# Kernel tuning notes

Hardware: AMD Instinct MI355X
Metric: run time of the kernel (lower is better)

The kernel has to match this reference:

```python
import jax, jax.numpy as jnp
import numpy as np

EMB, QK, V, H = 1024, 64, 64, 16
B, S = 4, 2048


def setup_inputs() -> dict:
    key = jax.random.key(0)
    ks = jax.random.split(key, 8)
    sc = 0.02
    x_q = jax.random.normal(ks[0], (B, S, EMB), jnp.float32)
    x_k_v = jax.random.normal(ks[1], (B, S, EMB), jnp.float32)
    # causal mask: True means masked (matches torch masked_fill)
    causal = ~jnp.tril(jnp.ones((S, S), dtype=bool))
    attn_mask = jnp.broadcast_to(causal, (B, S, S))
    w_q = jax.random.normal(ks[2], (H * QK, EMB), jnp.float32) * sc
    b_q = jnp.zeros((H * QK,), jnp.float32)
    w_k = jax.random.normal(ks[3], (H * QK, EMB), jnp.float32) * sc
    b_k = jnp.zeros((H * QK,), jnp.float32)
    w_v = jax.random.normal(ks[4], (H * V, EMB), jnp.float32) * sc
    b_v = jnp.zeros((H * V,), jnp.float32)
    return {"x_q": x_q, "x_k_v": x_k_v, "attn_mask": attn_mask,
            "w_q": w_q, "b_q": b_q, "w_k": w_k, "b_k": b_k, "w_v": w_v, "b_v": b_v}


def reference(x_q, x_k_v, attn_mask, w_q, b_q, w_k, b_k, w_v, b_v):
    Bq, Sq, _ = x_q.shape
    Skv = x_k_v.shape[1]
    q = (x_q @ w_q.T + b_q).reshape(Bq, Sq, H, QK).transpose(0, 2, 1, 3)   # [B,H,Sq,QK]
    k = (x_k_v @ w_k.T + b_k).reshape(Bq, Skv, H, QK).transpose(0, 2, 1, 3)  # [B,H,Skv,QK]
    v = (x_k_v @ w_v.T + b_v).reshape(Bq, Skv, H, V).transpose(0, 2, 1, 3)   # [B,H,Skv,V]
    attn = jnp.einsum('bhqd,bhkd->bhqk', q, k) / jnp.sqrt(jnp.float32(QK))
    attn = jnp.where(attn_mask[:, None, :, :], jnp.float32(-1e9), attn)
    attn = jax.nn.softmax(attn, axis=-1)
    z = jnp.einsum('bhqk,bhkv->bhqv', attn, v)        # [B,H,Sq,V]
    z = z.transpose(0, 2, 1, 3).reshape(Bq, Sq, H * V)
    return z
```

## Files before the change

kernel.cpp:

```cpp
#include <hip/hip_runtime.h>

#define B_    4
#define H_    16
#define S_    2048
#define EMB_  1024
#define D_    64

typedef __attribute__((ext_vector_type(4))) float f32x4;
typedef __attribute__((ext_vector_type(8))) short frag_ab;
typedef unsigned short ushort_t;

__device__ __forceinline__ unsigned short f2bf(float f) {
    unsigned int u = __float_as_uint(f);
    unsigned int r = u + 0x7fffu + ((u >> 16) & 1u);
    return (unsigned short)(r >> 16);
}
__device__ __forceinline__ unsigned short f2bf_fast(float f) {
    return (unsigned short)((__float_as_uint(f) + 0x8000u) >> 16);
}

__device__ __forceinline__ void gld16(const void* g, void* l) {
    __builtin_amdgcn_global_load_lds(
        (const __attribute__((address_space(1))) void*)g,
        (__attribute__((address_space(3))) void*)l, 16, 0, 0);
}

__global__ void cvt3_kernel(const float* __restrict__ s0, const float* __restrict__ s1,
                            const float* __restrict__ s2, ushort_t* __restrict__ d0,
                            ushort_t* __restrict__ d1, ushort_t* __restrict__ d2, int n4) {
    const float* src = (blockIdx.z == 0) ? s0 : (blockIdx.z == 1 ? s1 : s2);
    ushort_t* dst = (blockIdx.z == 0) ? d0 : (blockIdx.z == 1 ? d1 : d2);
    int i = blockIdx.x * blockDim.x + threadIdx.x;
    if (i >= n4) return;
    float4 f = ((const float4*)src)[i];
    ushort4 o;
    o.x = f2bf(f.x); o.y = f2bf(f.y); o.z = f2bf(f.z); o.w = f2bf(f.w);
    ((ushort4*)dst)[i] = o;
}
__global__ void cvt2_kernel(const float* __restrict__ s0, const float* __restrict__ s1,
                            ushort_t* __restrict__ d0, ushort_t* __restrict__ d1, int n4) {
    const float* src = (blockIdx.z == 0) ? s0 : s1;
    ushort_t* dst = (blockIdx.z == 0) ? d0 : d1;
    int i = blockIdx.x * blockDim.x + threadIdx.x;
    if (i >= n4) return;
    float4 f = ((const float4*)src)[i];
    ushort4 o;
    o.x = f2bf(f.x); o.y = f2bf(f.y); o.z = f2bf(f.z); o.w = f2bf(f.w);
    ((ushort4*)dst)[i] = o;
}

__global__ __launch_bounds__(256) void vtrans_kernel(
    const ushort_t* __restrict__ v, ushort_t* __restrict__ vt) {
    const int bh = blockIdx.y;
    const int s0 = blockIdx.x * 32 + (threadIdx.x >> 6) * 8;
    const int d  = threadIdx.x & 63;
    const ushort_t* vp = v + (size_t)bh * S_ * D_;
    ushort_t tmp[8];
#pragma unroll
    for (int j = 0; j < 8; ++j) tmp[j] = vp[(size_t)(s0 + j) * D_ + d];
    *(uint4*)&vt[(size_t)bh * D_ * S_ + (size_t)d * S_ + s0] = *(const uint4*)tmp;
}

__global__ __launch_bounds__(256) void qkv_gemm(
    const ushort_t* __restrict__ xq,
    const ushort_t* __restrict__ xkv,
    const ushort_t* __restrict__ wq,
    const ushort_t* __restrict__ wk,
    const ushort_t* __restrict__ wv,
    const float* __restrict__ bq,
    const float* __restrict__ bk,
    const float* __restrict__ bv,
    ushort_t* __restrict__ qo,
    ushort_t* __restrict__ ko,
    ushort_t* __restrict__ vo)
{
    __shared__ ushort_t As[2][128 * 32];
    __shared__ ushort_t Bs[2][128 * 32];

    const int z = blockIdx.z;
    const ushort_t* A = (z == 0) ? xq : xkv;
    const ushort_t* W = (z == 0) ? wq : (z == 1 ? wk : wv);
    const float* bias = (z == 0) ? bq : (z == 1 ? bk : bv);
    ushort_t* ob = (z == 0) ? qo : (z == 1 ? ko : vo);
    const float scale = (z == 0) ? 0.125f : 1.0f;

    const int tid = threadIdx.x;
    const int m0 = blockIdx.y * 128, n0 = blockIdx.x * 128;
    const int w = tid >> 6, lane = tid & 63, quad = lane >> 4, l16 = lane & 15;
    const int wm = w & 1, wn = w >> 1;
    const int row_in = lane >> 2, c8 = (lane & 3) * 8;

    f32x4 acc[4][4];
#pragma unroll
    for (int i = 0; i < 4; ++i)
#pragma unroll
        for (int j = 0; j < 4; ++j) acc[i][j] = (f32x4){0.f, 0.f, 0.f, 0.f};

    auto stage = [&](int b, int kt) {
        const int k0 = kt * 32;
#pragma unroll
        for (int i = 0; i < 2; ++i) {
            const int base = w * 32 + i * 16;
            gld16(A + (size_t)(m0 + base + row_in) * EMB_ + k0 + c8, &As[b][base * 32]);
            gld16(W + (size_t)(n0 + base + row_in) * EMB_ + k0 + c8, &Bs[b][base * 32]);
        }
    };

    stage(0, 0);
    for (int kt = 0; kt < 32; ++kt) {
        __syncthreads();
        if (kt < 31) stage((kt + 1) & 1, kt + 1);
        const int bsel = kt & 1;

        frag_ab a[4], bfr[4];
#pragma unroll
        for (int t = 0; t < 4; ++t) {
            a[t]   = *(const frag_ab*)&As[bsel][(wm * 64 + t * 16 + l16) * 32 + quad * 8];
            bfr[t] = *(const frag_ab*)&Bs[bsel][(wn * 64 + t * 16 + l16) * 32 + quad * 8];
        }
#pragma unroll
        for (int tm = 0; tm < 4; ++tm)
#pragma unroll
            for (int tn = 0; tn < 4; ++tn)
                acc[tm][tn] = __builtin_amdgcn_mfma_f32_16x16x32_bf16(
                    a[tm], bfr[tn], acc[tm][tn], 0, 0, 0);
    }

#pragma unroll
    for (int tn = 0; tn < 4; ++tn) {
        int n = n0 + wn * 64 + tn * 16 + l16;
        float bval = bias[n];
        int hh = n >> 6, dd = n & 63;
#pragma unroll
        for (int tm = 0; tm < 4; ++tm) {
#pragma unroll
            for (int r = 0; r < 4; ++r) {
                int m = m0 + wm * 64 + tm * 16 + quad * 4 + r;
                int bb = m >> 11, ss = m & (S_ - 1);
                float val = (acc[tm][tn][r] + bval) * scale;
                ob[(((size_t)bb * H_ + hh) * S_ + ss) * D_ + dd] = f2bf(val);
            }
        }
    }
}

#define LDP 72

__global__ __launch_bounds__(256) void attn_kernel(
    const ushort_t* __restrict__ qg,
    const ushort_t* __restrict__ kg,
    const ushort_t* __restrict__ vtg,
    float* __restrict__ out)
{
    __shared__ ushort_t Kt[2][2][64 * 32];
    __shared__ ushort_t Vt[2][2][64 * 32];
    __shared__ ushort_t Pb[4][32 * LDP];

    const int tid = threadIdx.x;
    const int w = tid >> 6, lane = tid & 63, quad = lane >> 4, l16 = lane & 15;
    const int row_in = lane >> 2, c8 = (lane & 3) * 8;

    const int id = blockIdx.x;
    const int rr = id >> 3;
    const int bh = (id & 7) + 8 * (rr & 7);
    const int qi = 15 - (rr >> 3);
    const int q0 = qi * 128;
    const int b = bh >> 4, h = bh & 15;

    const ushort_t* qp  = qg  + (size_t)bh * S_ * D_;
    const ushort_t* kp  = kg  + (size_t)bh * S_ * D_;
    const ushort_t* vtp = vtg + (size_t)bh * D_ * S_;

    frag_ab aq[2][2];
#pragma unroll
    for (int rg = 0; rg < 2; ++rg) {
        const ushort_t* qr = qp + (size_t)(q0 + rg * 64 + w * 16 + l16) * D_;
        aq[rg][0] = *(const frag_ab*)(qr + quad * 8);
        aq[rg][1] = *(const frag_ab*)(qr + 32 + quad * 8);
    }

    float psum[2][4];
    f32x4 o[2][4];
#pragma unroll
    for (int rg = 0; rg < 2; ++rg)
#pragma unroll
        for (int r = 0; r < 4; ++r) { psum[rg][r] = 0.f; }
#pragma unroll
    for (int rg = 0; rg < 2; ++rg)
#pragma unroll
        for (int t = 0; t < 4; ++t) o[rg][t] = (f32x4){0.f, 0.f, 0.f, 0.f};

    ushort_t* Pw = &Pb[w][0];
    const int last = 2 * qi + 1;

    auto stage = [&](int bsel, int kt) {
        const int base = w * 16;
        const ushort_t* kgp  = kp  + (size_t)(kt * 64 + base + row_in) * D_ + c8;
        const ushort_t* vtgp = vtp + (size_t)(base + row_in) * S_ + kt * 64 + c8;
        gld16(kgp,       &Kt[bsel][0][base * 32]);
        gld16(kgp + 32,  &Kt[bsel][1][base * 32]);
        gld16(vtgp,      &Vt[bsel][0][base * 32]);
        gld16(vtgp + 32, &Vt[bsel][1][base * 32]);
    };

    stage(0, 0);
    for (int kt = 0; kt <= last; ++kt) {
        __syncthreads();
        if (kt < last) stage((kt + 1) & 1, kt + 1);
        const int bsel = kt & 1;

        frag_ab bk[4][2], bv[4][2];
#pragma unroll
        for (int t = 0; t < 4; ++t) {
#pragma unroll
            for (int hf = 0; hf < 2; ++hf) {
                bk[t][hf] = *(const frag_ab*)&Kt[bsel][hf][(t * 16 + l16) * 32 + quad * 8];
                bv[t][hf] = *(const frag_ab*)&Vt[bsel][hf][(t * 16 + l16) * 32 + quad * 8];
            }
        }

#pragma unroll
        for (int rg = 0; rg < 2; ++rg) {
            if (rg == 0 && kt == last) continue;
            f32x4 scf[4];
#pragma unroll
            for (int tn = 0; tn < 4; ++tn) {
                f32x4 sc = (f32x4){0.f, 0.f, 0.f, 0.f};
                sc = __builtin_amdgcn_mfma_f32_16x16x32_bf16(aq[rg][0], bk[tn][0], sc, 0, 0, 0);
                sc = __builtin_amdgcn_mfma_f32_16x16x32_bf16(aq[rg][1], bk[tn][1], sc, 0, 0, 0);
                scf[tn] = sc;
            }
            if (kt == 2 * qi + rg) {
#pragma unroll
                for (int tn = 0; tn < 4; ++tn) {
                    int kcol = kt * 64 + tn * 16 + l16;
#pragma unroll
                    for (int r = 0; r < 4; ++r) {
                        int qrow = q0 + rg * 64 + w * 16 + quad * 4 + r;
                        if (kcol > qrow) scf[tn][r] = -1e30f;
                    }
                }
            }
#pragma unroll
            for (int tn = 0; tn < 4; ++tn) {
#pragma unroll
                for (int r = 0; r < 4; ++r) {
                    float p = __expf(scf[tn][r]);
                    psum[rg][r] += p;
                    Pw[(rg * 16 + quad * 4 + r) * LDP + tn * 16 + l16] = f2bf_fast(p);
                }
            }
        }
        asm volatile("s_waitcnt lgkmcnt(0)" ::: "memory");
#pragma unroll
        for (int rg = 0; rg < 2; ++rg) {
            if (rg == 0 && kt == last) continue;
            frag_ab ap0 = *(const frag_ab*)&Pw[(rg * 16 + l16) * LDP + quad * 8];
            frag_ab ap1 = *(const frag_ab*)&Pw[(rg * 16 + l16) * LDP + 32 + quad * 8];
#pragma unroll
            for (int tv = 0; tv < 4; ++tv) {
                o[rg][tv] = __builtin_amdgcn_mfma_f32_16x16x32_bf16(ap0, bv[tv][0], o[rg][tv], 0, 0, 0);
                o[rg][tv] = __builtin_amdgcn_mfma_f32_16x16x32_bf16(ap1, bv[tv][1], o[rg][tv], 0, 0, 0);
            }
        }
    }

    float* ob = out + (size_t)b * S_ * (H_ * D_) + h * D_;
#pragma unroll
    for (int rg = 0; rg < 2; ++rg) {
#pragma unroll
        for (int r = 0; r < 4; ++r) {
            float s = psum[rg][r];
            s += __shfl_xor(s, 1);
            s += __shfl_xor(s, 2);
            s += __shfl_xor(s, 4);
            s += __shfl_xor(s, 8);
            float inv = 1.0f / s;
            int srow = q0 + rg * 64 + w * 16 + quad * 4 + r;
#pragma unroll
            for (int tv = 0; tv < 4; ++tv)
                ob[(size_t)srow * (H_ * D_) + tv * 16 + l16] = o[rg][tv][r] * inv;
        }
    }
}

extern "C" void kernel_launch(void* const* d_in, const int* in_sizes, int n_in,
                              void* d_out, int out_size, void* d_ws, size_t ws_size,
                              hipStream_t stream) {
    const float* x_q  = (const float*)d_in[0];
    const float* x_kv = (const float*)d_in[1];
    const float* w_q  = (const float*)d_in[3];
    const float* b_q  = (const float*)d_in[4];
    const float* w_k  = (const float*)d_in[5];
    const float* b_k  = (const float*)d_in[6];
    const float* w_v  = (const float*)d_in[7];
    const float* b_v  = (const float*)d_in[8];
    float* out = (float*)d_out;

    ushort_t* ws  = (ushort_t*)d_ws;
    ushort_t* wqb = ws;
    ushort_t* wkb = wqb + 1048576;
    ushort_t* wvb = wkb + 1048576;
    ushort_t* xqb  = wvb + 1048576;
    ushort_t* xkvb = xqb + 8388608;
    ushort_t* qb   = xkvb + 8388608;
    ushort_t* kb   = qb + 8388608;
    ushort_t* vb   = kb + 8388608;
    ushort_t* vtb  = vb + 8388608;

    cvt3_kernel<<<dim3(1024, 1, 3), 256, 0, stream>>>(
        w_q, w_k, w_v, wqb, wkb, wvb, 262144);
    cvt2_kernel<<<dim3(8192, 1, 2), 256, 0, stream>>>(
        x_q, x_kv, xqb, xkvb, 2097152);
    qkv_gemm<<<dim3(8, 64, 3), 256, 0, stream>>>(
        xqb, xkvb, wqb, wkb, wvb, b_q, b_k, b_v, qb, kb, vb);
    vtrans_kernel<<<dim3(64, 64), 256, 0, stream>>>(vb, vtb);
    attn_kernel<<<1024, 256, 0, stream>>>(qb, kb, vtb, out);
}
```

Measured before the change: 321.4 us.

## Fuse conversions, write V transposed from GEMM, swizzle LDS, use exp2

Merges the two fp32-to-bf16 conversion kernels into one launch and removes the separate V transpose kernel by having the QKV GEMM epilogue write V directly in transposed layout. LDS fragments are XOR-swizzled in both the GEMM and attention kernels to cut bank conflicts, and the GEMM grid is remapped so tiles group by XCD for L2 reuse. The Q scale now folds in log2(e) so attention can use the hardware exp2. This removes two launches and a full V round trip through memory, at the cost of strided transposed stores in the GEMM epilogue and many oversized idle blocks in the merged conversion launch.

```diff
diff --git a/kernel.cpp b/kernel.cpp
--- a/kernel.cpp
+++ b/kernel.cpp
@@ -25,40 +25,30 @@
         (__attribute__((address_space(3))) void*)l, 16, 0, 0);
 }
 
-__global__ void cvt3_kernel(const float* __restrict__ s0, const float* __restrict__ s1,
-                            const float* __restrict__ s2, ushort_t* __restrict__ d0,
-                            ushort_t* __restrict__ d1, ushort_t* __restrict__ d2, int n4) {
-    const float* src = (blockIdx.z == 0) ? s0 : (blockIdx.z == 1 ? s1 : s2);
-    ushort_t* dst = (blockIdx.z == 0) ? d0 : (blockIdx.z == 1 ? d1 : d2);
+#define SWK(l16)  (((l16) >> 1) & 3)
+#define SWC(lane) ((((lane) & 3) ^ (((lane) >> 3) & 3)) * 8)
+
+__global__ void cvt_all(const float* __restrict__ s0, const float* __restrict__ s1,
+                        const float* __restrict__ s2, const float* __restrict__ s3,
+                        const float* __restrict__ s4,
+                        ushort_t* __restrict__ d0, ushort_t* __restrict__ d1,
+                        ushort_t* __restrict__ d2, ushort_t* __restrict__ d3,
+                        ushort_t* __restrict__ d4) {
+    const int z = blockIdx.z;
+    const float* src; ushort_t* dst; int n4;
+    switch (z) {
+        case 0: src = s0; dst = d0; n4 = 262144; break;
+        case 1: src = s1; dst = d1; n4 = 262144; break;
+        case 2: src = s2; dst = d2; n4 = 262144; break;
+        case 3: src = s3; dst = d3; n4 = 2097152; break;
+        default: src = s4; dst = d4; n4 = 2097152; break;
+    }
     int i = blockIdx.x * blockDim.x + threadIdx.x;
     if (i >= n4) return;
     float4 f = ((const float4*)src)[i];
     ushort4 o;
     o.x = f2bf(f.x); o.y = f2bf(f.y); o.z = f2bf(f.z); o.w = f2bf(f.w);
     ((ushort4*)dst)[i] = o;
-}
-__global__ void cvt2_kernel(const float* __restrict__ s0, const float* __restrict__ s1,
-                            ushort_t* __restrict__ d0, ushort_t* __restrict__ d1, int n4) {
-    const float* src = (blockIdx.z == 0) ? s0 : s1;
-    ushort_t* dst = (blockIdx.z == 0) ? d0 : d1;
-    int i = blockIdx.x * blockDim.x + threadIdx.x;
-    if (i >= n4) return;
-    float4 f = ((const float4*)src)[i];
-    ushort4 o;
-    o.x = f2bf(f.x); o.y = f2bf(f.y); o.z = f2bf(f.z); o.w = f2bf(f.w);
-    ((ushort4*)dst)[i] = o;
-}
-
-__global__ __launch_bounds__(256) void vtrans_kernel(
-    const ushort_t* __restrict__ v, ushort_t* __restrict__ vt) {
-    const int bh = blockIdx.y;
-    const int s0 = blockIdx.x * 32 + (threadIdx.x >> 6) * 8;
-    const int d  = threadIdx.x & 63;
-    const ushort_t* vp = v + (size_t)bh * S_ * D_;
-    ushort_t tmp[8];
-#pragma unroll
-    for (int j = 0; j < 8; ++j) tmp[j] = vp[(size_t)(s0 + j) * D_ + d];
-    *(uint4*)&vt[(size_t)bh * D_ * S_ + (size_t)d * S_ + s0] = *(const uint4*)tmp;
 }
 
 __global__ __launch_bounds__(256) void qkv_gemm(
@@ -72,40 +62,47 @@
     const float* __restrict__ bv,
     ushort_t* __restrict__ qo,
     ushort_t* __restrict__ ko,
-    ushort_t* __restrict__ vo)
+    ushort_t* __restrict__ vto)
 {
     __shared__ ushort_t As[2][128 * 32];
     __shared__ ushort_t Bs[2][128 * 32];
 
-    const int z = blockIdx.z;
+    const int id = blockIdx.x;
+    const int xcd = id & 7, j = id >> 3;
+    const int m_t = xcd * 8 + (j & 7);
+    const int n_t = (j >> 3) & 7;
+    const int z   = j >> 6;
+
     const ushort_t* A = (z == 0) ? xq : xkv;
     const ushort_t* W = (z == 0) ? wq : (z == 1 ? wk : wv);
     const float* bias = (z == 0) ? bq : (z == 1 ? bk : bv);
-    ushort_t* ob = (z == 0) ? qo : (z == 1 ? ko : vo);
-    const float scale = (z == 0) ? 0.125f : 1.0f;
+    const float scale = (z == 0) ? 0.125f * 1.44269504089f : 1.0f;
 
     const int tid = threadIdx.x;
-    const int m0 = blockIdx.y * 128, n0 = blockIdx.x * 128;
+    const int m0 = m_t * 128, n0 = n_t * 128;
     const int w = tid >> 6, lane = tid & 63, quad = lane >> 4, l16 = lane & 15;
     const int wm = w & 1, wn = w >> 1;
-    const int row_in = lane >> 2, c8 = (lane & 3) * 8;
+    const int row_in = lane >> 2, c8 = SWC(lane);
 
     f32x4 acc[4][4];
 #pragma unroll
     for (int i = 0; i < 4; ++i)
 #pragma unroll
-        for (int j = 0; j < 4; ++j) acc[i][j] = (f32x4){0.f, 0.f, 0.f, 0.f};
-
-    auto stage = [&](int b, int kt) {
+        for (int j2 = 0; j2 < 4; ++j2) acc[i][j2] = (f32x4){0.f, 0.f, 0.f, 0.f};
+
+    const ushort_t* pa = A + (size_t)(m0 + w * 32 + row_in) * EMB_ + c8;
+    const ushort_t* pw = W + (size_t)(n0 + w * 32 + row_in) * EMB_ + c8;
+
+    auto stage = [&](int bsel, int kt) {
         const int k0 = kt * 32;
-#pragma unroll
-        for (int i = 0; i < 2; ++i) {
-            const int base = w * 32 + i * 16;
-            gld16(A + (size_t)(m0 + base + row_in) * EMB_ + k0 + c8, &As[b][base * 32]);
-            gld16(W + (size_t)(n0 + base + row_in) * EMB_ + k0 + c8, &Bs[b][base * 32]);
-        }
+        const int base = w * 32;
+        gld16(pa + k0,             &As[bsel][base * 32]);
+        gld16(pa + 16 * EMB_ + k0, &As[bsel][(base + 16) * 32]);
+        gld16(pw + k0,             &Bs[bsel][base * 32]);
+        gld16(pw + 16 * EMB_ + k0, &Bs[bsel][(base + 16) * 32]);
     };
 
+    const int bq8 = (quad ^ SWK(l16)) * 8;
     stage(0, 0);
     for (int kt = 0; kt < 32; ++kt) {
         __syncthreads();
@@ -115,8 +112,8 @@
         frag_ab a[4], bfr[4];
 #pragma unroll
         for (int t = 0; t < 4; ++t) {
-            a[t]   = *(const frag_ab*)&As[bsel][(wm * 64 + t * 16 + l16) * 32 + quad * 8];
-            bfr[t] = *(const frag_ab*)&Bs[bsel][(wn * 64 + t * 16 + l16) * 32 + quad * 8];
+            a[t]   = *(const frag_ab*)&As[bsel][(wm * 64 + t * 16 + l16) * 32 + bq8];
+            bfr[t] = *(const frag_ab*)&Bs[bsel][(wn * 64 + t * 16 + l16) * 32 + bq8];
         }
 #pragma unroll
         for (int tm = 0; tm < 4; ++tm)
@@ -126,19 +123,38 @@
                     a[tm], bfr[tn], acc[tm][tn], 0, 0, 0);
     }
 
-#pragma unroll
-    for (int tn = 0; tn < 4; ++tn) {
-        int n = n0 + wn * 64 + tn * 16 + l16;
-        float bval = bias[n];
-        int hh = n >> 6, dd = n & 63;
-#pragma unroll
-        for (int tm = 0; tm < 4; ++tm) {
-#pragma unroll
-            for (int r = 0; r < 4; ++r) {
-                int m = m0 + wm * 64 + tm * 16 + quad * 4 + r;
+    if (z == 2) {
+#pragma unroll
+        for (int tn = 0; tn < 4; ++tn) {
+            int n = n0 + wn * 64 + tn * 16 + l16;
+            float bval = bias[n];
+            int hh = n >> 6, dd = n & 63;
+#pragma unroll
+            for (int tm = 0; tm < 4; ++tm) {
+                int m = m0 + wm * 64 + tm * 16 + quad * 4;
                 int bb = m >> 11, ss = m & (S_ - 1);
-                float val = (acc[tm][tn][r] + bval) * scale;
-                ob[(((size_t)bb * H_ + hh) * S_ + ss) * D_ + dd] = f2bf(val);
+                union { ushort4 v; ushort_t u[4]; } pk;
+#pragma unroll
+                for (int r = 0; r < 4; ++r) pk.u[r] = f2bf(acc[tm][tn][r] + bval);
+                *(ushort4*)&vto[(((size_t)bb * H_ + hh) * D_ + dd) * S_ + ss] = pk.v;
+            }
+        }
+    } else {
+        ushort_t* ob = (z == 0) ? qo : ko;
+#pragma unroll
+        for (int tn = 0; tn < 4; ++tn) {
+            int n = n0 + wn * 64 + tn * 16 + l16;
+            float bval = bias[n];
+            int hh = n >> 6, dd = n & 63;
+#pragma unroll
+            for (int tm = 0; tm < 4; ++tm) {
+#pragma unroll
+                for (int r = 0; r < 4; ++r) {
+                    int m = m0 + wm * 64 + tm * 16 + quad * 4 + r;
+                    int bb = m >> 11, ss = m & (S_ - 1);
+                    float val = (acc[tm][tn][r] + bval) * scale;
+                    ob[(((size_t)bb * H_ + hh) * S_ + ss) * D_ + dd] = f2bf(val);
+                }
             }
         }
     }
@@ -158,7 +174,7 @@
 
     const int tid = threadIdx.x;
     const int w = tid >> 6, lane = tid & 63, quad = lane >> 4, l16 = lane & 15;
-    const int row_in = lane >> 2, c8 = (lane & 3) * 8;
+    const int row_in = lane >> 2, c8 = SWC(lane);
 
     const int id = blockIdx.x;
     const int rr = id >> 3;
@@ -184,7 +200,7 @@
 #pragma unroll
     for (int rg = 0; rg < 2; ++rg)
 #pragma unroll
-        for (int r = 0; r < 4; ++r) { psum[rg][r] = 0.f; }
+        for (int r = 0; r < 4; ++r) psum[rg][r] = 0.f;
 #pragma unroll
     for (int rg = 0; rg < 2; ++rg)
 #pragma unroll
@@ -203,6 +219,7 @@
         gld16(vtgp + 32, &Vt[bsel][1][base * 32]);
     };
 
+    const int bq8 = (quad ^ SWK(l16)) * 8;
     stage(0, 0);
     for (int kt = 0; kt <= last; ++kt) {
         __syncthreads();
@@ -214,8 +231,8 @@
         for (int t = 0; t < 4; ++t) {
 #pragma unroll
             for (int hf = 0; hf < 2; ++hf) {
-                bk[t][hf] = *(const frag_ab*)&Kt[bsel][hf][(t * 16 + l16) * 32 + quad * 8];
-                bv[t][hf] = *(const frag_ab*)&Vt[bsel][hf][(t * 16 + l16) * 32 + quad * 8];
+                bk[t][hf] = *(const frag_ab*)&Kt[bsel][hf][(t * 16 + l16) * 32 + bq8];
+                bv[t][hf] = *(const frag_ab*)&Vt[bsel][hf][(t * 16 + l16) * 32 + bq8];
             }
         }
 
@@ -245,7 +262,7 @@
             for (int tn = 0; tn < 4; ++tn) {
 #pragma unroll
                 for (int r = 0; r < 4; ++r) {
-                    float p = __expf(scf[tn][r]);
+                    float p = __builtin_amdgcn_exp2f(scf[tn][r]);
                     psum[rg][r] += p;
                     Pw[(rg * 16 + quad * 4 + r) * LDP + tn * 16 + l16] = f2bf_fast(p);
                 }
@@ -305,15 +322,11 @@
     ushort_t* xkvb = xqb + 8388608;
     ushort_t* qb   = xkvb + 8388608;
     ushort_t* kb   = qb + 8388608;
-    ushort_t* vb   = kb + 8388608;
-    ushort_t* vtb  = vb + 8388608;
-
-    cvt3_kernel<<<dim3(1024, 1, 3), 256, 0, stream>>>(
-        w_q, w_k, w_v, wqb, wkb, wvb, 262144);
-    cvt2_kernel<<<dim3(8192, 1, 2), 256, 0, stream>>>(
-        x_q, x_kv, xqb, xkvb, 2097152);
-    qkv_gemm<<<dim3(8, 64, 3), 256, 0, stream>>>(
-        xqb, xkvb, wqb, wkb, wvb, b_q, b_k, b_v, qb, kb, vb);
-    vtrans_kernel<<<dim3(64, 64), 256, 0, stream>>>(vb, vtb);
+    ushort_t* vtb  = kb + 8388608;
+
+    cvt_all<<<dim3(8192, 1, 5), 256, 0, stream>>>(
+        w_q, w_k, w_v, x_q, x_kv, wqb, wkb, wvb, xqb, xkvb);
+    qkv_gemm<<<1536, 256, 0, stream>>>(
+        xqb, xkvb, wqb, wkb, wvb, b_q, b_k, b_v, qb, kb, vtb);
     attn_kernel<<<1024, 256, 0, stream>>>(qb, kb, vtb, out);
 }
```

Result: faster. 306.7 us (-4.6%).
